# Performance work log

Hardware: AMD Instinct MI355X
Metric: run time of the kernel (lower is better)

The kernel has to match this reference:

```python
import jax, jax.numpy as jnp
import numpy as np

EPS = 1.1920929e-07  # torch.finfo(float32).eps, used by nn.RMSNorm when eps=None
H = 16  # num_heads


def rmsnorm(x, w):
    return x * jax.lax.rsqrt(jnp.mean(x * x, axis=-1, keepdims=True) + EPS) * w


def attention(x, wq, wk, wv, wo, mask):
    # x: [b, s, d]; mask: [s, s] bool (True = attend)
    b, s, d = x.shape
    hd = d // H
    split = lambda t: t.reshape(b, s, H, hd).transpose(0, 2, 1, 3)  # b h s hd
    q, k, v = split(x @ wq), split(x @ wk), split(x @ wv)
    scale = 1.0 / float(np.sqrt(hd))
    scores = jnp.einsum('bhqd,bhkd->bhqk', q, k) * scale
    scores = jnp.where(mask, scores, jnp.asarray(-1e30, scores.dtype))
    p = jax.nn.softmax(scores, axis=-1)
    o = jnp.einsum('bhqk,bhkd->bhqd', p, v)
    return o.transpose(0, 2, 1, 3).reshape(b, s, d) @ wo


def setup_inputs() -> dict:
    key = jax.random.key(0)
    B, S, D, DFF = 2, 1024, 1024, 4096
    ks = jax.random.split(key, 32)
    w = lambda k, shape: jax.random.normal(k, shape, jnp.float32) * 0.02

    idx = jnp.arange(S)
    col_id = idx % 32            # COLUMN: interleaved column groups
    feat_id = idx // 128         # FEATURE: contiguous feature groups
    col_mask = col_id[:, None] == col_id[None, :]
    feat_mask = feat_id[:, None] == feat_id[None, :]
    nbr_mask = jnp.abs(idx[:, None] - idx[None, :]) <= 64  # NEIGHBOR: local band
    full_mask = jnp.ones((S, S), dtype=bool)

    return {
        'x': jax.random.normal(ks[0], (B, S, D), jnp.float32),
        'col_mask': col_mask, 'feat_mask': feat_mask,
        'nbr_mask': nbr_mask, 'full_mask': full_mask,
        'norm_c': jnp.ones((D,), jnp.float32), 'wq_c': w(ks[1], (D, D)), 'wk_c': w(ks[2], (D, D)), 'wv_c': w(ks[3], (D, D)), 'wo_c': w(ks[4], (D, D)),
        'norm_f': jnp.ones((D,), jnp.float32), 'wq_f': w(ks[5], (D, D)), 'wk_f': w(ks[6], (D, D)), 'wv_f': w(ks[7], (D, D)), 'wo_f': w(ks[8], (D, D)),
        'norm_n': jnp.ones((D,), jnp.float32), 'wq_n': w(ks[9], (D, D)), 'wk_n': w(ks[10], (D, D)), 'wv_n': w(ks[11], (D, D)), 'wo_n': w(ks[12], (D, D)),
        'norm_u': jnp.ones((D,), jnp.float32), 'wq_u': w(ks[13], (D, D)), 'wk_u': w(ks[14], (D, D)), 'wv_u': w(ks[15], (D, D)), 'wo_u': w(ks[16], (D, D)),
        'norm_ffn': jnp.ones((D,), jnp.float32), 'w_up': w(ks[17], (D, DFF)), 'w_gate': w(ks[18], (D, DFF)), 'w_down': w(ks[19], (DFF, D)),
    }


def reference(x, col_mask, feat_mask, nbr_mask, full_mask,
              norm_c, wq_c, wk_c, wv_c, wo_c,
              norm_f, wq_f, wk_f, wv_f, wo_f,
              norm_n, wq_n, wk_n, wv_n, wo_n,
              norm_u, wq_u, wk_u, wv_u, wo_u,
              norm_ffn, w_up, w_gate, w_down):
    x = x + attention(rmsnorm(x, norm_c), wq_c, wk_c, wv_c, wo_c, col_mask)
    x = x + attention(rmsnorm(x, norm_f), wq_f, wk_f, wv_f, wo_f, feat_mask)
    x = x + attention(rmsnorm(x, norm_n), wq_n, wk_n, wv_n, wo_n, nbr_mask)
    x = x + attention(rmsnorm(x, norm_u), wq_u, wk_u, wv_u, wo_u, full_mask)
    h = rmsnorm(x, norm_ffn)
    x = x + (jax.nn.silu(h @ w_gate) * (h @ w_up)) @ w_down  # SwiGLU FFN
    return x
```

## Files before the change

### kernel.cpp

```cpp
#include <hip/hip_runtime.h>
#include <math.h>
#include <stdint.h>


typedef __attribute__((ext_vector_type(8))) short bf16x8;
typedef __attribute__((ext_vector_type(4))) float f32x4;
typedef unsigned short ushort_t;
typedef unsigned int uint_t;

#define DEV static __device__ __forceinline__

DEV float bf2f(ushort_t u) { union { uint_t i; float f; } v; v.i = ((uint_t)u) << 16; return v.f; }
DEV ushort_t f2bf(float f) {
  union { float f; uint_t i; } v; v.f = f;
  uint_t r = v.i + 0x7fffu + ((v.i >> 16) & 1u);
  return (ushort_t)(r >> 16);
}
DEV uint_t pk2(ushort_t a, ushort_t b) { return (uint_t)a | ((uint_t)b << 16); }

DEV void gld16(const ushort_t* g, ushort_t* l) {
  __builtin_amdgcn_global_load_lds((const __attribute__((address_space(1))) void*)g,
                                   (__attribute__((address_space(3))) void*)l, 16, 0, 0);
}

struct Src16 { const float* p[16]; };

__global__ __launch_bounds__(256) void transpose16(Src16 s, ushort_t* __restrict__ qkvT,
                                                   ushort_t* __restrict__ woT) {
  __shared__ float tile[32][33];
  const int mz = blockIdx.z;
  const float* __restrict__ src = s.p[mz];
  const int l = mz >> 2, which = mz & 3;
  ushort_t* dst = (which < 3) ? (qkvT + (size_t)l*3072*1024 + (size_t)which*1024*1024)
                              : (woT  + (size_t)l*1024*1024);
  const int tx = threadIdx.x & 31, ty = threadIdx.x >> 5;
  const int r0 = blockIdx.y*32, c0 = blockIdx.x*32;
#pragma unroll
  for (int i = 0; i < 4; i++) tile[ty + 8*i][tx] = src[(size_t)(r0 + ty + 8*i)*1024 + c0 + tx];
  __syncthreads();
#pragma unroll
  for (int i = 0; i < 4; i++) dst[(size_t)(c0 + ty + 8*i)*1024 + r0 + tx] = f2bf(tile[tx][ty + 8*i]);
}

__global__ __launch_bounds__(256) void transpose_cvt(const float* __restrict__ src,
    ushort_t* __restrict__ dst, int R, int C, int row_off) {
  __shared__ float tile[32][33];
  const int tx = threadIdx.x & 31, ty = threadIdx.x >> 5;
  const int r0 = blockIdx.y*32, c0 = blockIdx.x*32;
#pragma unroll
  for (int i = 0; i < 4; i++) tile[ty + 8*i][tx] = src[(size_t)(r0 + ty + 8*i)*C + c0 + tx];
  __syncthreads();
#pragma unroll
  for (int i = 0; i < 4; i++)
    dst[(size_t)(row_off + c0 + ty + 8*i)*R + r0 + tx] = f2bf(tile[tx][ty + 8*i]);
}

template<int NS, int RMS>
__global__ __launch_bounds__(256) void fused_add_rms(
    const float* __restrict__ resid, const float* __restrict__ Pp,
    const float* __restrict__ w, float* __restrict__ xout,
    ushort_t* __restrict__ xn) {
  const int row = blockIdx.x, t = threadIdx.x;
  const size_t off = (size_t)row*1024 + t*4;
  float4 v = *(const float4*)&resid[off];
#pragma unroll
  for (int s = 0; s < NS; s++) {
    const float4 p = *(const float4*)&Pp[(size_t)s*(2048ull*1024) + off];
    v.x += p.x; v.y += p.y; v.z += p.z; v.w += p.w;
  }
  *(float4*)&xout[off] = v;
  if (RMS) {
    float ss = v.x*v.x + v.y*v.y + v.z*v.z + v.w*v.w;
#pragma unroll
    for (int m = 32; m; m >>= 1) ss += __shfl_xor(ss, m);
    __shared__ float red[4];
    if ((t & 63) == 0) red[t >> 6] = ss;
    __syncthreads();
    const float tot = red[0] + red[1] + red[2] + red[3];
    const float rs = rsqrtf(tot * (1.0f/1024.0f) + 1.1920929e-07f);
    const float4 wv = ((const float4*)w)[t];
    uint2 o;
    o.x = pk2(f2bf(v.x*rs*wv.x), f2bf(v.y*rs*wv.y));
    o.y = pk2(f2bf(v.z*rs*wv.z), f2bf(v.w*rs*wv.w));
    *(uint2*)&xn[off] = o;
  }
}

template<int BM, int BN, int EPI, int SPLITK>
__global__ __launch_bounds__(256, 4) void gemm_bt(
    const ushort_t* __restrict__ A, const ushort_t* __restrict__ BT,
    void* __restrict__ Cout, int M, int N, int K) {
  constexpr int BK = 64;
  __shared__ ushort_t Al[BM*BK];
  __shared__ ushort_t Bl[BN*BK];
  const int t = threadIdx.x, lane = t & 63;
  const int l15 = lane & 15, l4 = lane >> 4;
  int bid = blockIdx.y * gridDim.x + blockIdx.x;
  const int nwg = gridDim.x * gridDim.y;
  if ((nwg & 7) == 0) bid = (bid & 7) * (nwg >> 3) + (bid >> 3);
  const int n0 = (bid % gridDim.x) * BN;
  const int m0 = (bid / gridDim.x) * BM;
  constexpr int WM = BM/2, WN = BN/2, FM = WM/16, FN = WN/16;
  const int wm = ((t >> 6) >> 1) * WM;
  const int wn = ((t >> 6) & 1) * WN;
  const f32x4 zf = {0.f, 0.f, 0.f, 0.f};
  f32x4 acc[FM][FN];
#pragma unroll
  for (int m = 0; m < FM; m++)
#pragma unroll
    for (int n = 0; n < FN; n++) acc[m][n] = zf;
  constexpr int CA = (BM*BK)/(256*8), CB = (BN*BK)/(256*8);
  const int kz = blockIdx.z * (K / SPLITK);
  const int sw = l15 & 7;
  for (int k0 = kz; k0 < kz + K / SPLITK; k0 += BK) {
#pragma unroll
    for (int i = 0; i < CA; i++) {
      const int c = i*256 + t, row = c >> 3, ch = (c & 7) ^ (row & 7);
      gld16(&A[(size_t)(m0 + row)*K + k0 + ch*8], &Al[c*8]);
    }
#pragma unroll
    for (int i = 0; i < CB; i++) {
      const int c = i*256 + t, row = c >> 3, ch = (c & 7) ^ (row & 7);
      gld16(&BT[(size_t)(n0 + row)*K + k0 + ch*8], &Bl[c*8]);
    }
    __syncthreads();
#pragma unroll
    for (int kc = 0; kc < BK; kc += 32) {
      bf16x8 af[FM], bfr[FN];
#pragma unroll
      for (int m = 0; m < FM; m++)
        af[m] = *(const bf16x8*)&Al[(wm + m*16 + l15)*BK + (((kc >> 3) + l4) ^ sw)*8];
#pragma unroll
      for (int n = 0; n < FN; n++)
        bfr[n] = *(const bf16x8*)&Bl[(wn + n*16 + l15)*BK + (((kc >> 3) + l4) ^ sw)*8];
#pragma unroll
      for (int m = 0; m < FM; m++)
#pragma unroll
        for (int n = 0; n < FN; n++)
          acc[m][n] = __builtin_amdgcn_mfma_f32_16x16x32_bf16(af[m], bfr[n], acc[m][n], 0, 0, 0);
    }
    __syncthreads();
  }
#pragma unroll
  for (int m = 0; m < FM; m++)
#pragma unroll
    for (int n = 0; n < FN; n++)
#pragma unroll
      for (int r = 0; r < 4; r++) {
        const int row = m0 + wm + m*16 + l4*4 + r;
        const int col = n0 + wn + n*16 + l15;
        const size_t idx = (size_t)row*N + col;
        const float v = acc[m][n][r];
        if (EPI == 0) ((ushort_t*)Cout)[idx] = f2bf(v);
        else          ((float*)Cout)[(size_t)blockIdx.z*((size_t)M*N) + idx] = v;
      }
}

__global__ __launch_bounds__(256, 2) void gemm_gu_swiglu(
    const ushort_t* __restrict__ A, const ushort_t* __restrict__ BT,
    ushort_t* __restrict__ H) {
  constexpr int BK = 64;
  __shared__ ushort_t Al[128*BK];
  __shared__ ushort_t Bg[128*BK];
  __shared__ ushort_t Bu[128*BK];
  const int t = threadIdx.x, lane = t & 63;
  const int l15 = lane & 15, l4 = lane >> 4;
  int bid = blockIdx.y * gridDim.x + blockIdx.x;
  const int nwg = gridDim.x * gridDim.y;
  bid = (bid & 7) * (nwg >> 3) + (bid >> 3);
  const int n0 = (bid % gridDim.x) * 128;
  const int m0 = (bid / gridDim.x) * 128;
  const int wm = ((t >> 6) >> 1) * 64;
  const int wn = ((t >> 6) & 1) * 64;
  const f32x4 zf = {0.f, 0.f, 0.f, 0.f};
  f32x4 ag[4][4], au[4][4];
#pragma unroll
  for (int m = 0; m < 4; m++)
#pragma unroll
    for (int n = 0; n < 4; n++) { ag[m][n] = zf; au[m][n] = zf; }
  const int sw = l15 & 7;
  for (int k0 = 0; k0 < 1024; k0 += BK) {
#pragma unroll
    for (int i = 0; i < 4; i++) {
      const int c = i*256 + t, row = c >> 3, ch = (c & 7) ^ (row & 7);
      gld16(&A [(size_t)(m0 + row)*1024 + k0 + ch*8], &Al[c*8]);
      gld16(&BT[(size_t)(n0 + row)*1024 + k0 + ch*8], &Bg[c*8]);
      gld16(&BT[(size_t)(4096 + n0 + row)*1024 + k0 + ch*8], &Bu[c*8]);
    }
    __syncthreads();
#pragma unroll
    for (int kc = 0; kc < BK; kc += 32) {
      const int co = (((kc >> 3) + l4) ^ sw)*8;
      bf16x8 af[4], bgf[4], buf_[4];
#pragma unroll
      for (int m = 0; m < 4; m++) af[m]   = *(const bf16x8*)&Al[(wm + m*16 + l15)*BK + co];
#pragma unroll
      for (int n = 0; n < 4; n++) bgf[n]  = *(const bf16x8*)&Bg[(wn + n*16 + l15)*BK + co];
#pragma unroll
      for (int n = 0; n < 4; n++) buf_[n] = *(const bf16x8*)&Bu[(wn + n*16 + l15)*BK + co];
#pragma unroll
      for (int m = 0; m < 4; m++)
#pragma unroll
        for (int n = 0; n < 4; n++) {
          ag[m][n] = __builtin_amdgcn_mfma_f32_16x16x32_bf16(af[m], bgf[n], ag[m][n], 0, 0, 0);
          au[m][n] = __builtin_amdgcn_mfma_f32_16x16x32_bf16(af[m], buf_[n], au[m][n], 0, 0, 0);
        }
    }
    __syncthreads();
  }
#pragma unroll
  for (int m = 0; m < 4; m++)
#pragma unroll
    for (int n = 0; n < 4; n++)
#pragma unroll
      for (int r = 0; r < 4; r++) {
        const int row = m0 + wm + m*16 + l4*4 + r;
        const int col = n0 + wn + n*16 + l15;
        const float g = ag[m][n][r], u = au[m][n][r];
        H[(size_t)row*4096 + col] = f2bf(u * g / (1.0f + __expf(-g)));
      }
}

__global__ __launch_bounds__(256) void attn_col_k(const ushort_t* __restrict__ qkv,
                                                  ushort_t* __restrict__ O) {
  __shared__ float Qs[32][65], Ks[32][65], Vs[32][65], P[32][33];
  const int c = blockIdx.x, h = blockIdx.y, b = blockIdx.z, t = threadIdx.x;
  const size_t base = (size_t)b*1024*3072 + h*64;
  for (int e = t; e < 2048; e += 256) {
    const int u = e >> 6, d = e & 63;
    const size_t rb = base + (size_t)(c + 32*u)*3072 + d;
    Qs[u][d] = bf2f(qkv[rb]);
    Ks[u][d] = bf2f(qkv[rb + 1024]);
    Vs[u][d] = bf2f(qkv[rb + 2048]);
  }
  __syncthreads();
  const int u = t >> 3, kq = (t & 7)*4;
  float sc[4] = {0.f, 0.f, 0.f, 0.f};
  for (int d = 0; d < 64; d++) {
    const float q = Qs[u][d];
#pragma unroll
    for (int j = 0; j < 4; j++) sc[j] += q * Ks[kq + j][d];
  }
#pragma unroll
  for (int j = 0; j < 4; j++) P[u][kq + j] = __expf(sc[j] * 0.125f);
  __syncthreads();
  if (t < 32) {
    float sum = 0.f;
    for (int j = 0; j < 32; j++) sum += P[t][j];
    const float inv = 1.0f / sum;
    for (int j = 0; j < 32; j++) P[t][j] *= inv;
  }
  __syncthreads();
  const int dg = (t & 7)*8;
  float o[8] = {0.f,0.f,0.f,0.f,0.f,0.f,0.f,0.f};
  for (int k = 0; k < 32; k++) {
    const float p = P[u][k];
#pragma unroll
    for (int j = 0; j < 8; j++) o[j] += p * Vs[k][dg + j];
  }
  uint4 w4;
  w4.x = pk2(f2bf(o[0]), f2bf(o[1])); w4.y = pk2(f2bf(o[2]), f2bf(o[3]));
  w4.z = pk2(f2bf(o[4]), f2bf(o[5])); w4.w = pk2(f2bf(o[6]), f2bf(o[7]));
  *(uint4*)&O[(size_t)(b*1024 + c + 32*u)*1024 + h*64 + dg] = w4;
}

template<int MASK, int NSPLIT>
__global__ __launch_bounds__(256, 4) void attn_flash_k(const ushort_t* __restrict__ qkv,
    ushort_t* __restrict__ O, float* __restrict__ Opart, float* __restrict__ Lpart) {
  constexpr int LP = 66;
  __shared__ ushort_t Kl[64*LP];
  __shared__ ushort_t Vt[64*LP];
  __shared__ ushort_t Pl[4][16*LP];
  const int t = threadIdx.x, lane = t & 63, wave = t >> 6;
  const int l15 = lane & 15, l4 = lane >> 4;
  const int qt = blockIdx.x, h = blockIdx.y;
  const int b = blockIdx.z / NSPLIT, sp = blockIdx.z % NSPLIT;
  const int q0 = qt*64;
  const size_t base = (size_t)b*1024*3072 + h*64;
  const int qrow = q0 + wave*16 + l15;
  const bf16x8 qf0 = *(const bf16x8*)&qkv[base + (size_t)qrow*3072 + l4*8];
  const bf16x8 qf1 = *(const bf16x8*)&qkv[base + (size_t)qrow*3072 + 32 + l4*8];
  int klo, khi;
  if (MASK == 0)      { klo = q0 & ~127; khi = klo + 128; }
  else if (MASK == 1) { klo = (q0 >= 64) ? q0 - 64 : 0; khi = (q0 + 128 < 1024) ? q0 + 128 : 1024; }
  else                { klo = sp * (1024/NSPLIT); khi = klo + 1024/NSPLIT; }
  const int kr = t >> 2, kd = (t & 3)*16;
  const int vk2 = (t & 31)*2, vd = (t >> 5)*8;
  const ushort_t* kptr = qkv + base + 1024 + (size_t)kr*3072 + kd;
  const ushort_t* vptr = qkv + base + 2048 + (size_t)vk2*3072 + vd;
  bf16x8 kg0 = *(const bf16x8*)&kptr[(size_t)klo*3072];
  bf16x8 kg1 = *(const bf16x8*)&kptr[(size_t)klo*3072 + 8];
  bf16x8 vg0 = *(const bf16x8*)&vptr[(size_t)klo*3072];
  bf16x8 vg1 = *(const bf16x8*)&vptr[(size_t)klo*3072 + 3072];
  const f32x4 zf = {0.f, 0.f, 0.f, 0.f};
  f32x4 of[4];
#pragma unroll
  for (int n = 0; n < 4; n++) of[n] = zf;
  float lrow[4] = {0.f, 0.f, 0.f, 0.f};

  for (int kb = klo; kb < khi; kb += 64) {
    *(bf16x8*)&Kl[kr*LP + kd] = kg0;
    *(bf16x8*)&Kl[kr*LP + kd + 8] = kg1;
#pragma unroll
    for (int j = 0; j < 8; j++)
      *(uint_t*)&Vt[(vd + j)*LP + vk2] = pk2((ushort_t)vg0[j], (ushort_t)vg1[j]);
    __syncthreads();
    if (kb + 64 < khi) {
      kg0 = *(const bf16x8*)&kptr[(size_t)(kb+64)*3072];
      kg1 = *(const bf16x8*)&kptr[(size_t)(kb+64)*3072 + 8];
      vg0 = *(const bf16x8*)&vptr[(size_t)(kb+64)*3072];
      vg1 = *(const bf16x8*)&vptr[(size_t)(kb+64)*3072 + 3072];
    }
    f32x4 sf[4];
    __builtin_amdgcn_s_setprio(1);
#pragma unroll
    for (int s = 0; s < 4; s++) {
      const bf16x8 k0 = *(const bf16x8*)&Kl[(s*16 + l15)*LP + l4*8];
      const bf16x8 k1 = *(const bf16x8*)&Kl[(s*16 + l15)*LP + 32 + l4*8];
      sf[s] = __builtin_amdgcn_mfma_f32_16x16x32_bf16(qf0, k0, zf, 0, 0, 0);
      sf[s] = __builtin_amdgcn_mfma_f32_16x16x32_bf16(qf1, k1, sf[s], 0, 0, 0);
    }
    __builtin_amdgcn_s_setprio(0);
    float psum[4] = {0.f, 0.f, 0.f, 0.f};
#pragma unroll
    for (int s = 0; s < 4; s++)
#pragma unroll
      for (int r = 0; r < 4; r++) {
        float a = sf[s][r]*0.125f;
        if (MASK == 1) {
          const int d = (q0 + wave*16 + l4*4 + r) - (kb + s*16 + l15);
          if (d > 64 || d < -64) a = -1e30f;
        }
        const float p = __expf(a);
        psum[r] += p;
        Pl[wave][(l4*4 + r)*LP + s*16 + l15] = f2bf(p);
      }
#pragma unroll
    for (int mk = 1; mk < 16; mk <<= 1)
#pragma unroll
      for (int r = 0; r < 4; r++) psum[r] += __shfl_xor(psum[r], mk);
#pragma unroll
    for (int r = 0; r < 4; r++) lrow[r] += psum[r];
    const bf16x8 pa0 = *(const bf16x8*)&Pl[wave][l15*LP + l4*8];
    const bf16x8 pa1 = *(const bf16x8*)&Pl[wave][l15*LP + 32 + l4*8];
    __builtin_amdgcn_s_setprio(1);
#pragma unroll
    for (int n = 0; n < 4; n++) {
      const bf16x8 v0 = *(const bf16x8*)&Vt[(n*16 + l15)*LP + l4*8];
      const bf16x8 v1 = *(const bf16x8*)&Vt[(n*16 + l15)*LP + 32 + l4*8];
      of[n] = __builtin_amdgcn_mfma_f32_16x16x32_bf16(pa0, v0, of[n], 0, 0, 0);
      of[n] = __builtin_amdgcn_mfma_f32_16x16x32_bf16(pa1, v1, of[n], 0, 0, 0);
    }
    __builtin_amdgcn_s_setprio(0);
    __syncthreads();
  }
  if (NSPLIT == 1) {
#pragma unroll
    for (int n = 0; n < 4; n++)
#pragma unroll
      for (int r = 0; r < 4; r++) {
        const int qg = q0 + wave*16 + l4*4 + r;
        O[(size_t)(b*1024 + qg)*1024 + h*64 + n*16 + l15] = f2bf(of[n][r] / lrow[r]);
      }
  } else {
#pragma unroll
    for (int r = 0; r < 4; r++) {
      const int qg = q0 + wave*16 + l4*4 + r;
      const size_t row = ((size_t)(sp*2 + b)*1024 + qg)*16 + h;
#pragma unroll
      for (int n = 0; n < 4; n++) Opart[row*64 + n*16 + l15] = of[n][r];
      if (l15 == 0) Lpart[row] = lrow[r];
    }
  }
}

template<int NS>
__global__ __launch_bounds__(256) void attn_merge_k(const float* __restrict__ Opart,
    const float* __restrict__ L, ushort_t* __restrict__ O) {
  const int idx = blockIdx.x*256 + threadIdx.x;
  const int d8 = (idx & 7)*8;
  const int h  = (idx >> 3) & 15;
  const int q  = (idx >> 7) & 1023;
  const int b  = idx >> 17;
  float den = 0.f;
  float acc[8] = {0,0,0,0,0,0,0,0};
#pragma unroll
  for (int s = 0; s < NS; s++) {
    const size_t row = ((size_t)(s*2 + b)*1024 + q)*16 + h;
    den += L[row];
    const float4* op = (const float4*)&Opart[row*64 + d8];
    const float4 a = op[0], c = op[1];
    acc[0] += a.x; acc[1] += a.y; acc[2] += a.z; acc[3] += a.w;
    acc[4] += c.x; acc[5] += c.y; acc[6] += c.z; acc[7] += c.w;
  }
  const float inv = 1.0f / den;
  uint4 w4;
  w4.x = pk2(f2bf(acc[0]*inv), f2bf(acc[1]*inv));
  w4.y = pk2(f2bf(acc[2]*inv), f2bf(acc[3]*inv));
  w4.z = pk2(f2bf(acc[4]*inv), f2bf(acc[5]*inv));
  w4.w = pk2(f2bf(acc[6]*inv), f2bf(acc[7]*inv));
  *(uint4*)&O[((size_t)b*1024 + q)*1024 + h*64 + d8] = w4;
}

extern "C" void kernel_launch(void* const* d_in, const int* in_sizes, int n_in,
                              void* d_out, int out_size, void* d_ws, size_t ws_size,
                              hipStream_t stream) {
  (void)in_sizes; (void)n_in; (void)out_size; (void)ws_size;
  const float* x_in = (const float*)d_in[0];
  const float* norm[5] = { (const float*)d_in[5], (const float*)d_in[10], (const float*)d_in[15],
                           (const float*)d_in[20], (const float*)d_in[25] };
  char* w = (char*)d_ws;
  auto alloc = [&](size_t bytes) { char* p = w; w += (bytes + 255) & ~(size_t)255; return p; };
  ushort_t* qkvT = (ushort_t*)alloc(4ull*3072*1024*2);
  ushort_t* woT  = (ushort_t*)alloc(4ull*1024*1024*2);
  ushort_t* guT  = (ushort_t*)alloc(8192ull*1024*2);
  ushort_t* dnT  = (ushort_t*)alloc(4096ull*1024*2);
  float*    xbuf = (float*)  alloc(2048ull*1024*4);
  ushort_t* xn   = (ushort_t*)alloc(2048ull*1024*2);
  ushort_t* qkv  = (ushort_t*)alloc(2048ull*3072*2);
  ushort_t* attO = (ushort_t*)alloc(2048ull*1024*2);
  ushort_t* hmid = (ushort_t*)alloc(2048ull*4096*2);
  float*  scratch = (float*)alloc(8ull*1024*16*64*4);
  float* Pp    = scratch;
  float* Opart = scratch;
  float* Lpart = (float*)hmid;

  Src16 s;
  for (int l = 0; l < 4; l++) {
    s.p[l*4 + 0] = (const float*)d_in[6 + l*5];
    s.p[l*4 + 1] = (const float*)d_in[7 + l*5];
    s.p[l*4 + 2] = (const float*)d_in[8 + l*5];
    s.p[l*4 + 3] = (const float*)d_in[9 + l*5];
  }
  transpose16<<<dim3(32, 32, 16), 256, 0, stream>>>(s, qkvT, woT);
  transpose_cvt<<<dim3(128, 32), 256, 0, stream>>>((const float*)d_in[27], guT, 1024, 4096, 0);
  transpose_cvt<<<dim3(128, 32), 256, 0, stream>>>((const float*)d_in[26], guT, 1024, 4096, 4096);
  transpose_cvt<<<dim3(32, 128), 256, 0, stream>>>((const float*)d_in[28], dnT, 4096, 1024, 0);

  fused_add_rms<0,1><<<2048, 256, 0, stream>>>(x_in, nullptr, norm[0], xbuf, xn);

  for (int l = 0; l < 4; l++) {
    gemm_bt<64,192,0,1><<<dim3(3072/192, 2048/64), 256, 0, stream>>>(
        xn, qkvT + (size_t)l*3072*1024, qkv, 2048, 3072, 1024);
    if (l == 0)      attn_col_k         <<<dim3(32, 16, 2), 256, 0, stream>>>(qkv, attO);
    else if (l == 1) attn_flash_k<0,1>  <<<dim3(16, 16, 2), 256, 0, stream>>>(qkv, attO, nullptr, nullptr);
    else if (l == 2) attn_flash_k<1,1>  <<<dim3(16, 16, 2), 256, 0, stream>>>(qkv, attO, nullptr, nullptr);
    else {
      attn_flash_k<2,4><<<dim3(16, 16, 8), 256, 0, stream>>>(qkv, nullptr, Opart, Lpart);
      attn_merge_k<4><<<1024, 256, 0, stream>>>(Opart, Lpart, attO);
    }
    gemm_bt<128,64,3,2><<<dim3(1024/64, 2048/128, 2), 256, 0, stream>>>(
        attO, woT + (size_t)l*1024*1024, Pp, 2048, 1024, 1024);
    fused_add_rms<2,1><<<2048, 256, 0, stream>>>(xbuf, Pp, norm[l+1 < 4 ? l+1 : 4], xbuf, xn);
  }
  gemm_gu_swiglu<<<dim3(4096/128, 2048/128), 256, 0, stream>>>(xn, guT, hmid);
  gemm_bt<128,128,3,4><<<dim3(1024/128, 2048/128, 4), 256, 0, stream>>>(
      hmid, dnT, Pp, 2048, 1024, 4096);
  fused_add_rms<4,0><<<2048, 256, 0, stream>>>(xbuf, Pp, nullptr, (float*)d_out, nullptr);
}
```

Baseline: 506.5 us.

## Merge weight transposes into one launch and retune QKV and down-proj GEMM tiles

The four weight transpose/convert launches are merged into one flat-grid kernel that picks source, destination and shape from the block index. The QKV projection GEMM changes tile shape from 64x192 to 128x96. The down-projection GEMM moves from 128x128 tiles with split-K 4 to 128x64 tiles with split-K 2, and the final residual add now sums two partials instead of four. The goal is fewer launches, less partial-sum traffic and different occupancy, at the cost of more K-work per block in the down projection.

New measurement: 507.0 us. No clear change (+0.1%).

```diff
diff --git a/kernel.cpp b/kernel.cpp
--- a/kernel.cpp
+++ b/kernel.cpp
@@ -23,36 +23,40 @@
                                    (__attribute__((address_space(3))) void*)l, 16, 0, 0);
 }
 
-struct Src16 { const float* p[16]; };
-
-__global__ __launch_bounds__(256) void transpose16(Src16 s, ushort_t* __restrict__ qkvT,
-                                                   ushort_t* __restrict__ woT) {
+struct TPtrs { const float* src[19]; };
+
+__global__ __launch_bounds__(256) void transpose_all(TPtrs P, ushort_t* __restrict__ qkvT,
+    ushort_t* __restrict__ woT, ushort_t* __restrict__ guT, ushort_t* __restrict__ dnT) {
   __shared__ float tile[32][33];
-  const int mz = blockIdx.z;
-  const float* __restrict__ src = s.p[mz];
-  const int l = mz >> 2, which = mz & 3;
-  ushort_t* dst = (which < 3) ? (qkvT + (size_t)l*3072*1024 + (size_t)which*1024*1024)
-                              : (woT  + (size_t)l*1024*1024);
+  const int bid = blockIdx.x;
+  const float* src; ushort_t* dst; int C, R, bx, by;
+  if (bid < 16384) {
+    const int mz = bid >> 10, t10 = bid & 1023;
+    bx = t10 & 31; by = t10 >> 5;
+    src = P.src[mz]; R = 1024; C = 1024;
+    const int l = mz >> 2, which = mz & 3;
+    dst = (which < 3) ? (qkvT + (size_t)l*3072*1024 + (size_t)which*1024*1024)
+                      : (woT  + (size_t)l*1024*1024);
+  } else if (bid < 24576) {
+    const int seg = (bid - 16384) >> 12;
+    const int i = (bid - 16384) & 4095;
+    bx = i & 127; by = i >> 7;
+    src = P.src[16 + seg]; R = 1024; C = 4096;
+    dst = guT + (size_t)seg*4096*1024;
+  } else {
+    const int i = bid - 24576;
+    bx = i & 31; by = i >> 5;
+    src = P.src[18]; R = 4096; C = 1024;
+    dst = dnT;
+  }
   const int tx = threadIdx.x & 31, ty = threadIdx.x >> 5;
-  const int r0 = blockIdx.y*32, c0 = blockIdx.x*32;
-#pragma unroll
-  for (int i = 0; i < 4; i++) tile[ty + 8*i][tx] = src[(size_t)(r0 + ty + 8*i)*1024 + c0 + tx];
-  __syncthreads();
-#pragma unroll
-  for (int i = 0; i < 4; i++) dst[(size_t)(c0 + ty + 8*i)*1024 + r0 + tx] = f2bf(tile[tx][ty + 8*i]);
-}
-
-__global__ __launch_bounds__(256) void transpose_cvt(const float* __restrict__ src,
-    ushort_t* __restrict__ dst, int R, int C, int row_off) {
-  __shared__ float tile[32][33];
-  const int tx = threadIdx.x & 31, ty = threadIdx.x >> 5;
-  const int r0 = blockIdx.y*32, c0 = blockIdx.x*32;
+  const int r0 = by*32, c0 = bx*32;
 #pragma unroll
   for (int i = 0; i < 4; i++) tile[ty + 8*i][tx] = src[(size_t)(r0 + ty + 8*i)*C + c0 + tx];
   __syncthreads();
 #pragma unroll
   for (int i = 0; i < 4; i++)
-    dst[(size_t)(row_off + c0 + ty + 8*i)*R + r0 + tx] = f2bf(tile[tx][ty + 8*i]);
+    dst[(size_t)(c0 + ty + 8*i)*R + r0 + tx] = f2bf(tile[tx][ty + 8*i]);
 }
 
 template<int NS, int RMS>
@@ -425,22 +429,22 @@
   float* Opart = scratch;
   float* Lpart = (float*)hmid;
 
-  Src16 s;
+  TPtrs tp;
   for (int l = 0; l < 4; l++) {
-    s.p[l*4 + 0] = (const float*)d_in[6 + l*5];
-    s.p[l*4 + 1] = (const float*)d_in[7 + l*5];
-    s.p[l*4 + 2] = (const float*)d_in[8 + l*5];
-    s.p[l*4 + 3] = (const float*)d_in[9 + l*5];
-  }
-  transpose16<<<dim3(32, 32, 16), 256, 0, stream>>>(s, qkvT, woT);
-  transpose_cvt<<<dim3(128, 32), 256, 0, stream>>>((const float*)d_in[27], guT, 1024, 4096, 0);
-  transpose_cvt<<<dim3(128, 32), 256, 0, stream>>>((const float*)d_in[26], guT, 1024, 4096, 4096);
-  transpose_cvt<<<dim3(32, 128), 256, 0, stream>>>((const float*)d_in[28], dnT, 4096, 1024, 0);
+    tp.src[l*4 + 0] = (const float*)d_in[6 + l*5];
+    tp.src[l*4 + 1] = (const float*)d_in[7 + l*5];
+    tp.src[l*4 + 2] = (const float*)d_in[8 + l*5];
+    tp.src[l*4 + 3] = (const float*)d_in[9 + l*5];
+  }
+  tp.src[16] = (const float*)d_in[27];
+  tp.src[17] = (const float*)d_in[26];
+  tp.src[18] = (const float*)d_in[28];
+  transpose_all<<<28672, 256, 0, stream>>>(tp, qkvT, woT, guT, dnT);
 
   fused_add_rms<0,1><<<2048, 256, 0, stream>>>(x_in, nullptr, norm[0], xbuf, xn);
 
   for (int l = 0; l < 4; l++) {
-    gemm_bt<64,192,0,1><<<dim3(3072/192, 2048/64), 256, 0, stream>>>(
+    gemm_bt<128,96,0,1><<<dim3(3072/96, 2048/128), 256, 0, stream>>>(
         xn, qkvT + (size_t)l*3072*1024, qkv, 2048, 3072, 1024);
     if (l == 0)      attn_col_k         <<<dim3(32, 16, 2), 256, 0, stream>>>(qkv, attO);
     else if (l == 1) attn_flash_k<0,1>  <<<dim3(16, 16, 2), 256, 0, stream>>>(qkv, attO, nullptr, nullptr);
@@ -454,7 +458,7 @@
     fused_add_rms<2,1><<<2048, 256, 0, stream>>>(xbuf, Pp, norm[l+1 < 4 ? l+1 : 4], xbuf, xn);
   }
   gemm_gu_swiglu<<<dim3(4096/128, 2048/128), 256, 0, stream>>>(xn, guT, hmid);
-  gemm_bt<128,128,3,4><<<dim3(1024/128, 2048/128, 4), 256, 0, stream>>>(
+  gemm_bt<128,64,3,2><<<dim3(1024/64, 2048/128, 2), 256, 0, stream>>>(
       hmid, dnT, Pp, 2048, 1024, 4096);
-  fused_add_rms<4,0><<<2048, 256, 0, stream>>>(xbuf, Pp, nullptr, (float*)d_out, nullptr);
-}
+  fused_add_rms<2,0><<<2048, 256, 0, stream>>>(xbuf, Pp, nullptr, (float*)d_out, nullptr);
+}
```
